# Kernel tuning notes

Hardware: AMD Instinct MI355X
Metric: run time of the kernel (lower is better)

The kernel has to match this reference:

```python
import jax, jax.numpy as jnp
import numpy as np

D_FEAT, HID, N_LAYERS = 6, 64, 2
NEG_SLOPE = 0.01


def gru_layer(x_seq, W_ih, W_hh, b_ih, b_hh):
    # x_seq: [T, N, in]; PyTorch gate order r, z, n
    N = x_seq.shape[1]
    h0 = jnp.zeros((N, W_hh.shape[1]), x_seq.dtype)
    def step(h, x_t):
        gi = x_t @ W_ih.T + b_ih
        gh = h @ W_hh.T + b_hh
        i_r, i_z, i_n = jnp.split(gi, 3, axis=-1)
        h_r, h_z, h_n = jnp.split(gh, 3, axis=-1)
        r = jax.nn.sigmoid(i_r + h_r)
        z = jax.nn.sigmoid(i_z + h_z)
        n = jnp.tanh(i_n + r * h_n)
        h_new = (1.0 - z) * n + z * h
        return h_new, h_new
    _, ys = jax.lax.scan(step, h0, x_seq)
    return ys  # [T, N, H]


def setup_inputs() -> dict:
    key = jax.random.key(0)
    ks = jax.random.split(key, 16)
    N, T = 4000, 60
    x = jax.random.normal(ks[0], (N, D_FEAT * T), dtype=jnp.float32)
    relation_matrix = jax.random.randint(ks[1], (N, N, 8), 0, 2).astype(jnp.float32)
    s = 0.1
    p = {
        'W_ih0': jax.random.normal(ks[2], (3 * HID, D_FEAT), jnp.float32) * s,
        'W_hh0': jax.random.normal(ks[3], (3 * HID, HID), jnp.float32) * s,
        'b_ih0': jnp.zeros((3 * HID,), jnp.float32),
        'b_hh0': jnp.zeros((3 * HID,), jnp.float32),
        'W_ih1': jax.random.normal(ks[4], (3 * HID, HID), jnp.float32) * s,
        'W_hh1': jax.random.normal(ks[5], (3 * HID, HID), jnp.float32) * s,
        'b_ih1': jnp.zeros((3 * HID,), jnp.float32),
        'b_hh1': jnp.zeros((3 * HID,), jnp.float32),
        'W_0': jax.random.normal(ks[6], (2 * HID, 1), jnp.float32) * s,
        'b_0': jnp.zeros((), jnp.float32),
        'W_1': jax.random.normal(ks[7], (2 * HID, 1), jnp.float32) * s,
        'b_1': jnp.zeros((), jnp.float32),
        'W_2': jax.random.normal(ks[8], (2 * HID, 1), jnp.float32) * s,
        'b_2': jnp.zeros((), jnp.float32),
        'fc_w': jax.random.normal(ks[9], (1, 2 * HID), jnp.float32) * s,
        'fc_b': jnp.zeros((1,), jnp.float32),
    }
    return dict(x=x, relation_matrix=relation_matrix, **p)


def _head_softmax(h, W, b, mask):
    # weight[i,j] = leaky_relu(h_i @ W[:H] + h_j @ W[H:] + b); avoids [N,N,2H] concat
    H = h.shape[1]
    a = h @ W[:H]            # [N,1]
    c = h @ W[H:]            # [N,1]
    w = jax.nn.leaky_relu(a + c.T + b, NEG_SLOPE)  # [N,N]
    valid = jnp.where(mask == 0, -1000000.0, mask * w)
    return jax.nn.softmax(valid, axis=1)


def reference(x, relation_matrix, W_ih0, W_hh0, b_ih0, b_hh0, W_ih1, W_hh1, b_ih1, b_hh1,
              W_0, b_0, W_1, b_1, W_2, b_2, fc_w, fc_b):
    N = x.shape[0]
    xs = x.reshape(N, D_FEAT, -1).transpose(2, 0, 1)  # [T, N, d_feat]
    y1 = gru_layer(xs, W_ih0, W_hh0, b_ih0, b_hh0)
    y2 = gru_layer(y1, W_ih1, W_hh1, b_ih1, b_hh1)
    h = y2[-1]  # [N, H] last time step
    mask = jnp.sum(relation_matrix, axis=2)  # [N, N]
    s0 = _head_softmax(h, W_0, b_0, mask)
    s1 = _head_softmax(h, W_1, b_1, mask)
    s2 = _head_softmax(h, W_2, b_2, mask)
    agg = ((s0 + s1 + s2) / 3.0) @ h  # [N, H]
    hid = jnp.concatenate([h, agg], axis=1)  # [N, 2H]
    pred = (hid @ fc_w.T + fc_b).squeeze(-1)  # [N]
    return pred
```

## Files before the change

### kernel.cpp

```cpp
#include <hip/hip_runtime.h>

typedef __attribute__((ext_vector_type(8))) short bf16x8;
typedef __attribute__((ext_vector_type(4))) float f32x4;
typedef __attribute__((ext_vector_type(4))) float f4v;

__device__ __forceinline__ unsigned short f2bf(float f){
  unsigned u = __builtin_bit_cast(unsigned, f);
  u += 0x7FFFu + ((u >> 16) & 1u);
  return (unsigned short)(u >> 16);
}
__device__ __forceinline__ float bf2f(unsigned short b){
  unsigned u = ((unsigned)b) << 16;
  return __builtin_bit_cast(float, u);
}
__device__ __forceinline__ float sigmoidf_(float x){ return 1.f/(1.f + __expf(-x)); }
__device__ __forceinline__ float tanhf_(float x){
  float a = fabsf(x);
  float t = __expf(-2.f*a);
  float r = (1.f - t)/(1.f + t);
  return copysignf(r, x);
}

struct WF { bf16x8 hi, lo; };

__device__ __forceinline__ void mmsplit(bf16x8 ah, bf16x8 al, const WF& B,
                                        f32x4& Dh, f32x4& Dl){
  Dh = __builtin_amdgcn_mfma_f32_16x16x32_bf16(ah, B.hi, Dh, 0, 0, 0);
  Dl = __builtin_amdgcn_mfma_f32_16x16x32_bf16(al, B.hi, Dl, 0, 0, 0);
  Dl = __builtin_amdgcn_mfma_f32_16x16x32_bf16(ah, B.lo, Dl, 0, 0, 0);
}

__device__ __forceinline__ WF load_wf(const float* W, int ldk, int row, int k0, int kmax){
  WF f;
  #pragma unroll
  for (int j = 0; j < 8; j++){
    int k = k0 + j;
    float v = (k < kmax) ? W[row*ldk + k] : 0.f;
    unsigned short hb = f2bf(v);
    f.hi[j] = (short)hb;
    f.lo[j] = (short)f2bf(v - bf2f(hb));
  }
  return f;
}

__global__ __launch_bounds__(512, 2)
void gru_kernel(const float* __restrict__ x,
                const float* __restrict__ Wih0, const float* __restrict__ Whh0,
                const float* __restrict__ bih0, const float* __restrict__ bhh0,
                const float* __restrict__ Wih1, const float* __restrict__ Whh1,
                const float* __restrict__ bih1, const float* __restrict__ bhh1,
                float* __restrict__ hfin){
  __shared__ unsigned short xp_hi[16][60][8];
  __shared__ unsigned short xp_lo[16][60][8];
  __shared__ unsigned short h0hi[2][16][72], h0lo[2][16][72];
  __shared__ unsigned short h1hi[2][16][72], h1lo[2][16][72];

  const int tid  = threadIdx.x;
  const int lane = tid & 63;
  const int wv   = tid >> 6;
  const bool isA = (wv < 4);
  const int w    = wv & 3;
  const int c    = lane & 15;
  const int q    = lane >> 4;
  const int d    = w*16 + c;
  const int nbase = blockIdx.x * 16;

  for (int v = tid; v < 16*360; v += 512){
    int n = v / 360, rem = v % 360;
    int dd = rem / 60, tt = rem % 60;
    float f = x[(size_t)(nbase + n)*360 + rem];
    unsigned short hb = f2bf(f);
    xp_hi[n][tt][dd] = hb;
    xp_lo[n][tt][dd] = f2bf(f - bf2f(hb));
  }
  for (int v = tid; v < 16*60*2; v += 512){
    int n = v / 120, rem = v % 120;
    int tt = rem >> 1, dd = 6 + (rem & 1);
    xp_hi[n][tt][dd] = 0; xp_lo[n][tt][dd] = 0;
  }
  for (int v = tid; v < 2*16*72; v += 512){
    ((unsigned short*)h0hi)[v] = 0; ((unsigned short*)h0lo)[v] = 0;
    ((unsigned short*)h1hi)[v] = 0; ((unsigned short*)h1lo)[v] = 0;
  }

  const float* bib = isA ? bih0 : bih1;
  const float* bhb = isA ? bhh0 : bhh1;
  const float bir = bib[d], biz = bib[64+d], bin = bib[128+d];
  const float bhr = bhb[d], bhz = bhb[64+d], bhn = bhb[128+d];

  WF Bu[3][2], Bv[3][2];
  #pragma unroll
  for (int g = 0; g < 3; g++){
    int row = g*64 + d;
    if (isA){
      Bu[g][0] = load_wf(Wih0, 6, row, q*8, 6);
      Bu[g][1] = Bu[g][0];
      #pragma unroll
      for (int kt = 0; kt < 2; kt++)
        Bv[g][kt] = load_wf(Whh0, 64, row, kt*32 + q*8, 64);
    } else {
      #pragma unroll
      for (int kt = 0; kt < 2; kt++){
        Bu[g][kt] = load_wf(Wih1, 64, row, kt*32 + q*8, 64);
        Bv[g][kt] = load_wf(Whh1, 64, row, kt*32 + q*8, 64);
      }
    }
  }

  float hold[4] = {0,0,0,0};

  auto stepB = [&](int s){
    const int rb = (s + 1) & 1;
    const int sb = s & 1;
    bf16x8 ayh[2], ayl[2], ahh[2], ahl[2];
    #pragma unroll
    for (int kt = 0; kt < 2; kt++){
      ayh[kt] = *(const bf16x8*)&h0hi[rb][c][kt*32 + q*8];
      ayl[kt] = *(const bf16x8*)&h0lo[rb][c][kt*32 + q*8];
      ahh[kt] = *(const bf16x8*)&h1hi[sb][c][kt*32 + q*8];
      ahl[kt] = *(const bf16x8*)&h1lo[sb][c][kt*32 + q*8];
    }
    f32x4 RH = {0,0,0,0}, RL = {0,0,0,0};
    f32x4 ZH = {0,0,0,0}, ZL = {0,0,0,0};
    f32x4 NIH = {0,0,0,0}, NIL = {0,0,0,0};
    f32x4 NHH = {0,0,0,0}, NHL = {0,0,0,0};
    #pragma unroll
    for (int kt = 0; kt < 2; kt++){
      mmsplit(ayh[kt], ayl[kt], Bu[0][kt], RH, RL);
      mmsplit(ayh[kt], ayl[kt], Bu[1][kt], ZH, ZL);
      mmsplit(ayh[kt], ayl[kt], Bu[2][kt], NIH, NIL);
      mmsplit(ahh[kt], ahl[kt], Bv[0][kt], RH, RL);
      mmsplit(ahh[kt], ahl[kt], Bv[1][kt], ZH, ZL);
      mmsplit(ahh[kt], ahl[kt], Bv[2][kt], NHH, NHL);
    }
    #pragma unroll
    for (int rI = 0; rI < 4; rI++){
      float rv = sigmoidf_(RH[rI] + RL[rI] + bir + bhr);
      float zv = sigmoidf_(ZH[rI] + ZL[rI] + biz + bhz);
      float nv = tanhf_(NIH[rI] + NIL[rI] + bin + rv*(NHH[rI] + NHL[rI] + bhn));
      float hnew = (1.f - zv)*nv + zv*hold[rI];
      hold[rI] = hnew;
      unsigned short hb = f2bf(hnew);
      int node = q*4 + rI;
      h1hi[rb][node][d] = hb;
      h1lo[rb][node][d] = f2bf(hnew - bf2f(hb));
    }
  };

  __syncthreads();

  #pragma unroll 1
  for (int t = 0; t < 60; t++){
    if (isA){
      const int p  = t & 1;
      const int nb = p ^ 1;
      bf16x8 ah[2], al[2];
      #pragma unroll
      for (int kt = 0; kt < 2; kt++){
        ah[kt] = *(const bf16x8*)&h0hi[p][c][kt*32 + q*8];
        al[kt] = *(const bf16x8*)&h0lo[p][c][kt*32 + q*8];
      }
      bf16x8 axh = {}, axl = {};
      if (q == 0){
        axh = *(const bf16x8*)&xp_hi[c][t][0];
        axl = *(const bf16x8*)&xp_lo[c][t][0];
      }
      f32x4 RH = {0,0,0,0}, RL = {0,0,0,0};
      f32x4 ZH = {0,0,0,0}, ZL = {0,0,0,0};
      f32x4 NIH = {0,0,0,0}, NIL = {0,0,0,0};
      f32x4 NHH = {0,0,0,0}, NHL = {0,0,0,0};
      mmsplit(axh, axl, Bu[0][0], RH, RL);
      mmsplit(axh, axl, Bu[1][0], ZH, ZL);
      mmsplit(axh, axl, Bu[2][0], NIH, NIL);
      #pragma unroll
      for (int kt = 0; kt < 2; kt++){
        mmsplit(ah[kt], al[kt], Bv[0][kt], RH, RL);
        mmsplit(ah[kt], al[kt], Bv[1][kt], ZH, ZL);
        mmsplit(ah[kt], al[kt], Bv[2][kt], NHH, NHL);
      }
      #pragma unroll
      for (int rI = 0; rI < 4; rI++){
        float rv = sigmoidf_(RH[rI] + RL[rI] + bir + bhr);
        float zv = sigmoidf_(ZH[rI] + ZL[rI] + biz + bhz);
        float nv = tanhf_(NIH[rI] + NIL[rI] + bin + rv*(NHH[rI] + NHL[rI] + bhn));
        float hnew = (1.f - zv)*nv + zv*hold[rI];
        hold[rI] = hnew;
        unsigned short hb = f2bf(hnew);
        int node = q*4 + rI;
        h0hi[nb][node][d] = hb;
        h0lo[nb][node][d] = f2bf(hnew - bf2f(hb));
      }
    } else if (t > 0){
      stepB(t - 1);
    }
    __syncthreads();
  }

  if (!isA){
    stepB(59);
    #pragma unroll
    for (int rI = 0; rI < 4; rI++){
      int node = nbase + q*4 + rI;
      hfin[(size_t)node*64 + d] = hold[rI];
    }
  }
}

__global__ void ac_kernel(const float* __restrict__ hfin,
                          const float* __restrict__ W0h, const float* __restrict__ W1h,
                          const float* __restrict__ W2h, float* __restrict__ ac){
  int lane = threadIdx.x & 63;
  int node = blockIdx.x*4 + (threadIdx.x >> 6);
  float hv = hfin[(size_t)node*64 + lane];
  const float* Ws[3] = {W0h, W1h, W2h};
  #pragma unroll
  for (int h = 0; h < 3; h++){
    float pa = hv * Ws[h][lane];
    float pc = hv * Ws[h][64 + lane];
    #pragma unroll
    for (int m = 32; m >= 1; m >>= 1){
      pa += __shfl_xor(pa, m, 64);
      pc += __shfl_xor(pc, m, 64);
    }
    if (lane == 0){
      ac[(size_t)(2*h)*4000 + node]   = pa;
      ac[(size_t)(2*h+1)*4000 + node] = pc;
    }
  }
}

__global__ __launch_bounds__(256, 4)
void attn2_kernel(const float* __restrict__ rel, const float* __restrict__ hfin,
                  const float* __restrict__ ac,
                  const float* __restrict__ b0p, const float* __restrict__ b1p,
                  const float* __restrict__ b2p,
                  const float* __restrict__ fcw, const float* __restrict__ fcb,
                  float* __restrict__ pred){
  __shared__ float m0[4000], m1[4000];
  __shared__ float red[4][8];

  const int tid  = threadIdx.x;
  const int lane = tid & 63;
  const int w    = tid >> 6;
  const int i0   = blockIdx.x * 2;
  const float bh[3] = {b0p[0], b1p[0], b2p[0]};

  const float* c0 = ac + 1*4000;
  const float* c1 = ac + 3*4000;
  const float* c2 = ac + 5*4000;

  float ai[2][3];
  #pragma unroll
  for (int r = 0; r < 2; r++)
    #pragma unroll
    for (int h = 0; h < 3; h++)
      ai[r][h] = ac[(size_t)(2*h)*4000 + i0 + r];

  float z[2][3] = {{0.f,0.f,0.f},{0.f,0.f,0.f}};

  {
    const size_t base0 = (size_t)i0*4000;
    const size_t base1 = (size_t)(i0+1)*4000;
    int j = tid;
    bool h0 = (j < 4000);
    bool h1 = (j + 256 < 4000);
    f4v a0, a1, a2, a3, b0, b1, b2, b3;
    if (h0){
      const f4v* rp0 = (const f4v*)(rel + (base0 + j)*8);
      const f4v* rp1 = (const f4v*)(rel + (base1 + j)*8);
      a0 = __builtin_nontemporal_load(rp0);
      a1 = __builtin_nontemporal_load(rp0 + 1);
      a2 = __builtin_nontemporal_load(rp1);
      a3 = __builtin_nontemporal_load(rp1 + 1);
    }
    if (h1){
      const f4v* rp0 = (const f4v*)(rel + (base0 + j + 256)*8);
      const f4v* rp1 = (const f4v*)(rel + (base1 + j + 256)*8);
      b0 = __builtin_nontemporal_load(rp0);
      b1 = __builtin_nontemporal_load(rp0 + 1);
      b2 = __builtin_nontemporal_load(rp1);
      b3 = __builtin_nontemporal_load(rp1 + 1);
    }
    while (h0){
      int j2 = j + 512;
      bool h2 = (j2 < 4000);
      f4v c0v, c1v, c2v, c3v;
      if (h2){
        const f4v* rp0 = (const f4v*)(rel + (base0 + j2)*8);
        const f4v* rp1 = (const f4v*)(rel + (base1 + j2)*8);
        c0v = __builtin_nontemporal_load(rp0);
        c1v = __builtin_nontemporal_load(rp0 + 1);
        c2v = __builtin_nontemporal_load(rp1);
        c3v = __builtin_nontemporal_load(rp1 + 1);
      }
      float mk0 = a0[0]+a0[1]+a0[2]+a0[3] + a1[0]+a1[1]+a1[2]+a1[3];
      float mk1 = a2[0]+a2[1]+a2[2]+a2[3] + a3[0]+a3[1]+a3[2]+a3[3];
      m0[j] = mk0; m1[j] = mk1;
      float cv[3] = {c0[j], c1[j], c2[j]};
      #pragma unroll
      for (int h = 0; h < 3; h++){
        float s0 = ai[0][h] + cv[h] + bh[h];
        float s1 = ai[1][h] + cv[h] + bh[h];
        float w0 = s0 > 0.f ? s0 : 0.01f*s0;
        float w1 = s1 > 0.f ? s1 : 0.01f*s1;
        float v0 = (mk0 == 0.f) ? -1e6f : mk0*w0;
        float v1 = (mk1 == 0.f) ? -1e6f : mk1*w1;
        z[0][h] += __expf(v0);
        z[1][h] += __expf(v1);
      }
      a0 = b0; a1 = b1; a2 = b2; a3 = b3;
      b0 = c0v; b1 = c1v; b2 = c2v; b3 = c3v;
      j += 256; h0 = h1; h1 = h2;
    }
  }
  #pragma unroll
  for (int r = 0; r < 2; r++)
    #pragma unroll
    for (int h = 0; h < 3; h++){
      float v = z[r][h];
      #pragma unroll
      for (int m = 32; m >= 1; m >>= 1) v += __shfl_xor(v, m, 64);
      if (lane == 0) red[w][r*3 + h] = v;
    }
  __syncthreads();
  float iZ[2][3];
  #pragma unroll
  for (int r = 0; r < 2; r++)
    #pragma unroll
    for (int h = 0; h < 3; h++)
      iZ[r][h] = 1.f/(red[0][r*3+h] + red[1][r*3+h] + red[2][r*3+h] + red[3][r*3+h]);

  for (int j = tid; j < 4000; j += 256){
    float mk0 = m0[j], mk1 = m1[j];
    float cv[3] = {c0[j], c1[j], c2[j]};
    float w0s = 0.f, w1s = 0.f;
    #pragma unroll
    for (int h = 0; h < 3; h++){
      float s0 = ai[0][h] + cv[h] + bh[h];
      float s1 = ai[1][h] + cv[h] + bh[h];
      float w0 = s0 > 0.f ? s0 : 0.01f*s0;
      float w1 = s1 > 0.f ? s1 : 0.01f*s1;
      float v0 = (mk0 == 0.f) ? -1e6f : mk0*w0;
      float v1 = (mk1 == 0.f) ? -1e6f : mk1*w1;
      w0s += __expf(v0) * iZ[0][h];
      w1s += __expf(v1) * iZ[1][h];
    }
    m0[j] = w0s * (1.f/3.f);
    m1[j] = w1s * (1.f/3.f);
  }
  __syncthreads();

  float acc0 = 0.f, acc1 = 0.f;
  const int jb = w * 1000;
  for (int jj = 0; jj < 1000; jj += 4){
    float4 w0 = *(const float4*)&m0[jb + jj];
    float4 w1 = *(const float4*)&m1[jb + jj];
    float w0a[4] = {w0.x, w0.y, w0.z, w0.w};
    float w1a[4] = {w1.x, w1.y, w1.z, w1.w};
    #pragma unroll
    for (int k = 0; k < 4; k++){
      float hv = hfin[(size_t)(jb + jj + k)*64 + lane];
      acc0 = fmaf(w0a[k], hv, acc0);
      acc1 = fmaf(w1a[k], hv, acc1);
    }
  }
  __syncthreads();
  m0[(w*2 + 0)*64 + lane] = acc0;
  m0[(w*2 + 1)*64 + lane] = acc1;
  __syncthreads();
  if (tid < 128){
    int r = tid >> 6, d = tid & 63;
    float agg = m0[(0*2+r)*64 + d] + m0[(1*2+r)*64 + d]
              + m0[(2*2+r)*64 + d] + m0[(3*2+r)*64 + d];
    float term = hfin[(size_t)(i0+r)*64 + d]*fcw[d] + agg*fcw[64 + d];
    #pragma unroll
    for (int m = 32; m >= 1; m >>= 1) term += __shfl_xor(term, m, 64);
    if (d == 0) pred[i0 + r] = term + fcb[0];
  }
}

extern "C" void kernel_launch(void* const* d_in, const int* in_sizes, int n_in,
                              void* d_out, int out_size, void* d_ws, size_t ws_size,
                              hipStream_t stream) {
  const float* x    = (const float*)d_in[0];
  const float* rel  = (const float*)d_in[1];
  const float* Wih0 = (const float*)d_in[2];
  const float* Whh0 = (const float*)d_in[3];
  const float* bih0 = (const float*)d_in[4];
  const float* bhh0 = (const float*)d_in[5];
  const float* Wih1 = (const float*)d_in[6];
  const float* Whh1 = (const float*)d_in[7];
  const float* bih1 = (const float*)d_in[8];
  const float* bhh1 = (const float*)d_in[9];
  const float* W0   = (const float*)d_in[10];
  const float* b0   = (const float*)d_in[11];
  const float* W1   = (const float*)d_in[12];
  const float* b1   = (const float*)d_in[13];
  const float* W2   = (const float*)d_in[14];
  const float* b2   = (const float*)d_in[15];
  const float* fcw  = (const float*)d_in[16];
  const float* fcb  = (const float*)d_in[17];
  float* pred = (float*)d_out;
  float* hfin = (float*)d_ws;
  float* ac   = hfin + 4000*64;

  gru_kernel<<<dim3(250), dim3(512), 0, stream>>>(x, Wih0, Whh0, bih0, bhh0,
                                                  Wih1, Whh1, bih1, bhh1, hfin);
  ac_kernel<<<dim3(1000), dim3(256), 0, stream>>>(hfin, W0, W1, W2, ac);
  attn2_kernel<<<dim3(2000), dim3(256), 0, stream>>>(rel, hfin, ac, b0, b1, b2,
                                                     fcw, fcb, pred);
}
```

Baseline: 860.2 us.

## Fold fc projection into attention to compute scalar weighted sums in one pass

Projects each node's hidden state onto the fc weights ahead of time, so the attention kernel only accumulates exp-weighted sums of a scalar per neighbour alongside the softmax normaliser. This removes the second exp pass, the shared-memory weight arrays and the per-block weighted sum over all hidden vectors. It relies on reassociating the softmax normalisation and fc dot product, which changes floating-point summation order.

```diff
diff --git a/kernel.cpp b/kernel.cpp
--- a/kernel.cpp
+++ b/kernel.cpp
@@ -208,7 +208,9 @@
 
 __global__ void ac_kernel(const float* __restrict__ hfin,
                           const float* __restrict__ W0h, const float* __restrict__ W1h,
-                          const float* __restrict__ W2h, float* __restrict__ ac){
+                          const float* __restrict__ W2h,
+                          const float* __restrict__ fcw, const float* __restrict__ fcb,
+                          float* __restrict__ ac){
   int lane = threadIdx.x & 63;
   int node = blockIdx.x*4 + (threadIdx.x >> 6);
   float hv = hfin[(size_t)node*64 + lane];
@@ -227,17 +229,24 @@
       ac[(size_t)(2*h+1)*4000 + node] = pc;
     }
   }
+  float pg = hv * fcw[64 + lane];
+  float pp = hv * fcw[lane];
+  #pragma unroll
+  for (int m = 32; m >= 1; m >>= 1){
+    pg += __shfl_xor(pg, m, 64);
+    pp += __shfl_xor(pp, m, 64);
+  }
+  if (lane == 0){
+    ac[(size_t)6*4000 + node] = pg;
+    ac[(size_t)7*4000 + node] = pp + fcb[0];
+  }
 }
 
 __global__ __launch_bounds__(256, 4)
-void attn2_kernel(const float* __restrict__ rel, const float* __restrict__ hfin,
-                  const float* __restrict__ ac,
+void attn2_kernel(const float* __restrict__ rel, const float* __restrict__ ac,
                   const float* __restrict__ b0p, const float* __restrict__ b1p,
-                  const float* __restrict__ b2p,
-                  const float* __restrict__ fcw, const float* __restrict__ fcb,
-                  float* __restrict__ pred){
-  __shared__ float m0[4000], m1[4000];
-  __shared__ float red[4][8];
+                  const float* __restrict__ b2p, float* __restrict__ pred){
+  __shared__ float red[4][12];
 
   const int tid  = threadIdx.x;
   const int lane = tid & 63;
@@ -245,9 +254,11 @@
   const int i0   = blockIdx.x * 2;
   const float bh[3] = {b0p[0], b1p[0], b2p[0]};
 
-  const float* c0 = ac + 1*4000;
-  const float* c1 = ac + 3*4000;
-  const float* c2 = ac + 5*4000;
+  const float* c0 = ac + (size_t)1*4000;
+  const float* c1 = ac + (size_t)3*4000;
+  const float* c2 = ac + (size_t)5*4000;
+  const float* gv = ac + (size_t)6*4000;
+  const float* p0 = ac + (size_t)7*4000;
 
   float ai[2][3];
   #pragma unroll
@@ -257,15 +268,16 @@
       ai[r][h] = ac[(size_t)(2*h)*4000 + i0 + r];
 
   float z[2][3] = {{0.f,0.f,0.f},{0.f,0.f,0.f}};
+  float y[2][3] = {{0.f,0.f,0.f},{0.f,0.f,0.f}};
 
   {
     const size_t base0 = (size_t)i0*4000;
     const size_t base1 = (size_t)(i0+1)*4000;
     int j = tid;
-    bool h0 = (j < 4000);
-    bool h1 = (j + 256 < 4000);
+    bool hv0 = (j < 4000);
+    bool hv1 = (j + 256 < 4000);
     f4v a0, a1, a2, a3, b0, b1, b2, b3;
-    if (h0){
+    if (hv0){
       const f4v* rp0 = (const f4v*)(rel + (base0 + j)*8);
       const f4v* rp1 = (const f4v*)(rel + (base1 + j)*8);
       a0 = __builtin_nontemporal_load(rp0);
@@ -273,7 +285,7 @@
       a2 = __builtin_nontemporal_load(rp1);
       a3 = __builtin_nontemporal_load(rp1 + 1);
     }
-    if (h1){
+    if (hv1){
       const f4v* rp0 = (const f4v*)(rel + (base0 + j + 256)*8);
       const f4v* rp1 = (const f4v*)(rel + (base1 + j + 256)*8);
       b0 = __builtin_nontemporal_load(rp0);
@@ -281,22 +293,22 @@
       b2 = __builtin_nontemporal_load(rp1);
       b3 = __builtin_nontemporal_load(rp1 + 1);
     }
-    while (h0){
+    while (hv0){
       int j2 = j + 512;
-      bool h2 = (j2 < 4000);
-      f4v c0v, c1v, c2v, c3v;
-      if (h2){
+      bool hv2 = (j2 < 4000);
+      f4v n0, n1, n2, n3;
+      if (hv2){
         const f4v* rp0 = (const f4v*)(rel + (base0 + j2)*8);
         const f4v* rp1 = (const f4v*)(rel + (base1 + j2)*8);
-        c0v = __builtin_nontemporal_load(rp0);
-        c1v = __builtin_nontemporal_load(rp0 + 1);
-        c2v = __builtin_nontemporal_load(rp1);
-        c3v = __builtin_nontemporal_load(rp1 + 1);
+        n0 = __builtin_nontemporal_load(rp0);
+        n1 = __builtin_nontemporal_load(rp0 + 1);
+        n2 = __builtin_nontemporal_load(rp1);
+        n3 = __builtin_nontemporal_load(rp1 + 1);
       }
       float mk0 = a0[0]+a0[1]+a0[2]+a0[3] + a1[0]+a1[1]+a1[2]+a1[3];
       float mk1 = a2[0]+a2[1]+a2[2]+a2[3] + a3[0]+a3[1]+a3[2]+a3[3];
-      m0[j] = mk0; m1[j] = mk1;
       float cv[3] = {c0[j], c1[j], c2[j]};
+      float gj = gv[j];
       #pragma unroll
       for (int h = 0; h < 3; h++){
         float s0 = ai[0][h] + cv[h] + bh[h];
@@ -305,77 +317,43 @@
         float w1 = s1 > 0.f ? s1 : 0.01f*s1;
         float v0 = (mk0 == 0.f) ? -1e6f : mk0*w0;
         float v1 = (mk1 == 0.f) ? -1e6f : mk1*w1;
-        z[0][h] += __expf(v0);
-        z[1][h] += __expf(v1);
+        float e0 = __expf(v0);
+        float e1 = __expf(v1);
+        z[0][h] += e0;  y[0][h] = fmaf(e0, gj, y[0][h]);
+        z[1][h] += e1;  y[1][h] = fmaf(e1, gj, y[1][h]);
       }
       a0 = b0; a1 = b1; a2 = b2; a3 = b3;
-      b0 = c0v; b1 = c1v; b2 = c2v; b3 = c3v;
-      j += 256; h0 = h1; h1 = h2;
-    }
-  }
+      b0 = n0; b1 = n1; b2 = n2; b3 = n3;
+      j += 256; hv0 = hv1; hv1 = hv2;
+    }
+  }
+
   #pragma unroll
   for (int r = 0; r < 2; r++)
     #pragma unroll
     for (int h = 0; h < 3; h++){
-      float v = z[r][h];
-      #pragma unroll
-      for (int m = 32; m >= 1; m >>= 1) v += __shfl_xor(v, m, 64);
-      if (lane == 0) red[w][r*3 + h] = v;
+      float vz = z[r][h], vy = y[r][h];
+      #pragma unroll
+      for (int m = 32; m >= 1; m >>= 1){
+        vz += __shfl_xor(vz, m, 64);
+        vy += __shfl_xor(vy, m, 64);
+      }
+      if (lane == 0){
+        red[w][(r*3 + h)*2 + 0] = vz;
+        red[w][(r*3 + h)*2 + 1] = vy;
+      }
     }
   __syncthreads();
-  float iZ[2][3];
-  #pragma unroll
-  for (int r = 0; r < 2; r++)
-    #pragma unroll
-    for (int h = 0; h < 3; h++)
-      iZ[r][h] = 1.f/(red[0][r*3+h] + red[1][r*3+h] + red[2][r*3+h] + red[3][r*3+h]);
-
-  for (int j = tid; j < 4000; j += 256){
-    float mk0 = m0[j], mk1 = m1[j];
-    float cv[3] = {c0[j], c1[j], c2[j]};
-    float w0s = 0.f, w1s = 0.f;
+  if (tid < 2){
+    int r = tid;
+    float acc = 0.f;
     #pragma unroll
     for (int h = 0; h < 3; h++){
-      float s0 = ai[0][h] + cv[h] + bh[h];
-      float s1 = ai[1][h] + cv[h] + bh[h];
-      float w0 = s0 > 0.f ? s0 : 0.01f*s0;
-      float w1 = s1 > 0.f ? s1 : 0.01f*s1;
-      float v0 = (mk0 == 0.f) ? -1e6f : mk0*w0;
-      float v1 = (mk1 == 0.f) ? -1e6f : mk1*w1;
-      w0s += __expf(v0) * iZ[0][h];
-      w1s += __expf(v1) * iZ[1][h];
-    }
-    m0[j] = w0s * (1.f/3.f);
-    m1[j] = w1s * (1.f/3.f);
-  }
-  __syncthreads();
-
-  float acc0 = 0.f, acc1 = 0.f;
-  const int jb = w * 1000;
-  for (int jj = 0; jj < 1000; jj += 4){
-    float4 w0 = *(const float4*)&m0[jb + jj];
-    float4 w1 = *(const float4*)&m1[jb + jj];
-    float w0a[4] = {w0.x, w0.y, w0.z, w0.w};
-    float w1a[4] = {w1.x, w1.y, w1.z, w1.w};
-    #pragma unroll
-    for (int k = 0; k < 4; k++){
-      float hv = hfin[(size_t)(jb + jj + k)*64 + lane];
-      acc0 = fmaf(w0a[k], hv, acc0);
-      acc1 = fmaf(w1a[k], hv, acc1);
-    }
-  }
-  __syncthreads();
-  m0[(w*2 + 0)*64 + lane] = acc0;
-  m0[(w*2 + 1)*64 + lane] = acc1;
-  __syncthreads();
-  if (tid < 128){
-    int r = tid >> 6, d = tid & 63;
-    float agg = m0[(0*2+r)*64 + d] + m0[(1*2+r)*64 + d]
-              + m0[(2*2+r)*64 + d] + m0[(3*2+r)*64 + d];
-    float term = hfin[(size_t)(i0+r)*64 + d]*fcw[d] + agg*fcw[64 + d];
-    #pragma unroll
-    for (int m = 32; m >= 1; m >>= 1) term += __shfl_xor(term, m, 64);
-    if (d == 0) pred[i0 + r] = term + fcb[0];
+      float zz = red[0][(r*3+h)*2] + red[1][(r*3+h)*2] + red[2][(r*3+h)*2] + red[3][(r*3+h)*2];
+      float yy = red[0][(r*3+h)*2+1] + red[1][(r*3+h)*2+1] + red[2][(r*3+h)*2+1] + red[3][(r*3+h)*2+1];
+      acc += yy / zz;
+    }
+    pred[i0 + r] = p0[i0 + r] + acc * (1.f/3.f);
   }
 }
 
@@ -406,7 +384,6 @@
 
   gru_kernel<<<dim3(250), dim3(512), 0, stream>>>(x, Wih0, Whh0, bih0, bhh0,
                                                   Wih1, Whh1, bih1, bhh1, hfin);
-  ac_kernel<<<dim3(1000), dim3(256), 0, stream>>>(hfin, W0, W1, W2, ac);
-  attn2_kernel<<<dim3(2000), dim3(256), 0, stream>>>(rel, hfin, ac, b0, b1, b2,
-                                                     fcw, fcb, pred);
-}
+  ac_kernel<<<dim3(1000), dim3(256), 0, stream>>>(hfin, W0, W1, W2, fcw, fcb, ac);
+  attn2_kernel<<<dim3(2000), dim3(256), 0, stream>>>(rel, ac, b0, b1, b2, pred);
+}
```

New measurement: 778.4 us. 9.5% less time.
